# Kernel optimization log

Hardware: AMD Instinct MI355X
Metric: run time of the kernel (lower is better)

Reference implementation:

```python
import jax, jax.numpy as jnp
import numpy as np

EPS = 1e-6

def setup_inputs() -> dict:
    key = jax.random.key(0)
    k1, k2, k3 = jax.random.split(key, 3)
    N, L, S, H, D = 8, 4096, 4096, 8, 64
    queries = jax.random.normal(k1, (N, L, H, D), dtype=jnp.float32)
    keys = jax.random.normal(k2, (N, S, H, D), dtype=jnp.float32)
    values = jax.random.normal(k3, (N, S, H, D), dtype=jnp.float32)
    return {"queries": queries, "keys": keys, "values": values}

def reference(queries, keys, values):
    # elu(x)+1 feature maps (positive kernel)
    Q = jax.nn.elu(queries) + 1.0  # [N,L,H,D]
    K = jax.nn.elu(keys) + 1.0     # [N,S,H,D]
    v_length = values.shape[1]
    v = values / v_length          # scale for numerical stability
    # per-head KV state: [N,H,D,Dv]
    KV = jnp.einsum('nshd,nshv->nhdv', K, v)
    # normalizer: [N,L,H]
    K_sum = K.sum(axis=1)  # [N,H,D]
    Z = 1.0 / (jnp.einsum('nlhd,nhd->nlh', Q, K_sum) + EPS)
    out = jnp.einsum('nlhd,nhdv,nlh->nlhv', Q, KV, Z) * v_length
    return out
```

## Files before the change

### kernel.cpp

```cpp
#include <hip/hip_runtime.h>
#include <hip/hip_bf16.h>
#include <cstddef>
#include <cstdint>

#define N_B   8
#define L_L   4096
#define S_S   4096
#define H_H   8
#define D_D   64
#define NH    64
#define KVLD  68
#define KVSZ  (65 * KVLD)

typedef const float __attribute__((address_space(1)))* gas_fp;
typedef float __attribute__((address_space(3)))* las_fp;

__device__ __forceinline__ float elu1(float x) {
    return x > 0.f ? x + 1.f : __expf(x);
}

__global__ __launch_bounds__(256, 4)
void la_phase1(const float* __restrict__ Kin, const float* __restrict__ Vin,
               float* __restrict__ partials, int split, int schunk)
{
    __shared__ union {
        struct { float K[32 * 64]; float V[2][32 * 64]; } st;
        float acc[64 * 68];
    } sm;
    __shared__ float sKsumP[4 * 64];

    const int b     = blockIdx.x;
    const int nh    = b / split;
    const int chunk = b - nh * split;
    const int n     = nh >> 3;
    const int h     = nh & 7;
    const int s0    = chunk * schunk;

    const int tid  = threadIdx.x;
    const int w    = tid >> 6;
    const int lane = tid & 63;
    const int dg   = lane >> 3;
    const int vg   = lane & 7;

    float acc[8][8];
    #pragma unroll
    for (int i = 0; i < 8; ++i)
        #pragma unroll
        for (int j = 0; j < 8; ++j) acc[i][j] = 0.f;
    float ksum = 0.f;

    const int kd = lane;

    const int lrow = lane >> 4;
    const int lcol = (lane & 15) * 4;

    const float* Kb = Kin + (size_t)n * S_S * (H_H * D_D) + h * D_D;
    const float* Vb = Vin + (size_t)n * S_S * (H_H * D_D) + h * D_D;

    const int ntiles = schunk >> 5;

    #pragma unroll
    for (int c = 0; c < 2; ++c) {
        const int r = w * 8 + c * 4 + lrow;
        __builtin_amdgcn_global_load_lds(
            (gas_fp)(Vb + (size_t)(s0 + r) * (H_H * D_D) + lcol),
            (las_fp)&sm.st.V[0][(w * 8 + c * 4) * 64], 16, 0, 0);
    }

    for (int t = 0; t < ntiles; ++t) {
        const int srow = s0 + t * 32;

        #pragma unroll
        for (int c = 0; c < 2; ++c) {
            const int r = w * 8 + c * 4 + lrow;
            float4 kv = *(const float4*)(Kb + (size_t)(srow + r) * (H_H * D_D) + lcol);
            kv.x = elu1(kv.x); kv.y = elu1(kv.y);
            kv.z = elu1(kv.z); kv.w = elu1(kv.w);
            *(float4*)&sm.st.K[(w * 8 + c * 4) * 64 + lane * 4] = kv;
        }

        if (t + 1 < ntiles) {
            const int srn = srow + 32;
            #pragma unroll
            for (int c = 0; c < 2; ++c) {
                const int r = w * 8 + c * 4 + lrow;
                __builtin_amdgcn_global_load_lds(
                    (gas_fp)(Vb + (size_t)(srn + r) * (H_H * D_D) + lcol),
                    (las_fp)&sm.st.V[(t & 1) ^ 1][(w * 8 + c * 4) * 64], 16, 0, 0);
            }
            asm volatile("s_waitcnt vmcnt(2)" ::: "memory");
        } else {
            asm volatile("s_waitcnt vmcnt(0)" ::: "memory");
        }

        const float* Kbuf = sm.st.K;
        const float* Vbuf = sm.st.V[t & 1];

        #pragma unroll
        for (int sl = 0; sl < 8; ++sl) {
            const int s = w * 8 + sl;
            const float4 k0 = *(const float4*)&Kbuf[s * 64 + dg * 8];
            const float4 k1 = *(const float4*)&Kbuf[s * 64 + dg * 8 + 4];
            const float4 v0 = *(const float4*)&Vbuf[s * 64 + vg * 8];
            const float4 v1 = *(const float4*)&Vbuf[s * 64 + vg * 8 + 4];
            const float kf[8] = {k0.x, k0.y, k0.z, k0.w, k1.x, k1.y, k1.z, k1.w};
            const float vf[8] = {v0.x, v0.y, v0.z, v0.w, v1.x, v1.y, v1.z, v1.w};
            #pragma unroll
            for (int i = 0; i < 8; ++i)
                #pragma unroll
                for (int j = 0; j < 8; ++j)
                    acc[i][j] = fmaf(kf[i], vf[j], acc[i][j]);
        }
        #pragma unroll
        for (int sl = 0; sl < 8; ++sl)
            ksum += Kbuf[(w * 8 + sl) * 64 + kd];
    }
    __syncthreads();

    for (int ww = 0; ww < 4; ++ww) {
        if (w == ww) {
            #pragma unroll
            for (int i = 0; i < 8; ++i) {
                float* p = &sm.acc[(dg * 8 + i) * 68 + vg * 8];
                if (ww == 0) {
                    *(float4*)p       = make_float4(acc[i][0], acc[i][1], acc[i][2], acc[i][3]);
                    *(float4*)(p + 4) = make_float4(acc[i][4], acc[i][5], acc[i][6], acc[i][7]);
                } else {
                    float4 a0 = *(const float4*)p;
                    float4 a1 = *(const float4*)(p + 4);
                    a0.x += acc[i][0]; a0.y += acc[i][1]; a0.z += acc[i][2]; a0.w += acc[i][3];
                    a1.x += acc[i][4]; a1.y += acc[i][5]; a1.z += acc[i][6]; a1.w += acc[i][7];
                    *(float4*)p       = a0;
                    *(float4*)(p + 4) = a1;
                }
            }
        }
        __syncthreads();
    }

    sKsumP[w * 64 + kd] = ksum;
    __syncthreads();

    float* outp = partials + (size_t)b * KVSZ;
    for (int idx = tid; idx < KVSZ; idx += 256) {
        const int r = idx / KVLD;
        const int c = idx - r * KVLD;
        float val = 0.f;
        if (c < 64) {
            if (r < 64)
                val = sm.acc[idx];
            else
                val = sKsumP[c] + sKsumP[64 + c] + sKsumP[128 + c] + sKsumP[192 + c];
        }
        outp[idx] = val;
    }
}

__global__ __launch_bounds__(256)
void la_reduce(const float* __restrict__ partials, float* __restrict__ kvt, int split)
{
    const int idx = blockIdx.x * 256 + threadIdx.x;
    if (idx >= NH * KVSZ) return;
    const int nh  = idx / KVSZ;
    const int rem = idx - nh * KVSZ;
    const float* p = partials + (size_t)nh * split * KVSZ + rem;
    float s = 0.f;
    for (int c = 0; c < split; ++c) s += p[(size_t)c * KVSZ];
    kvt[idx] = s;
}

__global__ __launch_bounds__(256, 2)
void la_phase2(const float* __restrict__ Qin, const float* __restrict__ kvt,
               float* __restrict__ Out)
{
    __shared__ float sQ[128 * 68];
    __shared__ float sKV[KVSZ];

    const int b   = blockIdx.x;
    const int nh  = b >> 5;
    const int lc  = b & 31;
    const int n   = nh >> 3;
    const int h   = nh & 7;
    const int tid = threadIdx.x;
    const int w    = tid >> 6;
    const int lane = tid & 63;

    const float* Qc = Qin + (((size_t)n * L_L + (size_t)lc * 128) * H_H + h) * D_D;
    float*       Oc = Out + (((size_t)n * L_L + (size_t)lc * 128) * H_H + h) * D_D;

    {
        const float4* src = (const float4*)(kvt + (size_t)nh * KVSZ);
        float4*       dst = (float4*)sKV;
        #pragma unroll
        for (int it = 0; it < 4; ++it)
            dst[it * 256 + tid] = src[it * 256 + tid];
        if (tid < 81) dst[1024 + tid] = src[1024 + tid];
    }

    #pragma unroll
    for (int it = 0; it < 8; ++it) {
        const int slot = it * 256 + tid;
        const int r    = slot >> 4;
        const int c4   = slot & 15;
        float4 v = *(const float4*)(Qc + (size_t)r * (H_H * D_D) + c4 * 4);
        v.x = elu1(v.x); v.y = elu1(v.y); v.z = elu1(v.z); v.w = elu1(v.w);
        *(float4*)&sQ[r * 68 + c4 * 4] = v;
    }
    __syncthreads();

    const int rt   = (w >> 1) * 64;
    const int wc   = w & 1;
    const int rl   = lane & 7;
    const int cg   = lane >> 3;
    const int ccol = wc * 32 + cg * 4;

    float acc[8][4];
    float den[8];
    #pragma unroll
    for (int j = 0; j < 8; ++j) {
        den[j] = 0.f;
        #pragma unroll
        for (int m = 0; m < 4; ++m) acc[j][m] = 0.f;
    }

    const int qbase = rt + rl;

    for (int kc = 0; kc < 16; ++kc) {
        float4 qv[8];
        #pragma unroll
        for (int j = 0; j < 8; ++j)
            qv[j] = *(const float4*)&sQ[(qbase + 8 * j) * 68 + kc * 4];
        const float4 kv0 = *(const float4*)&sKV[(kc * 4 + 0) * KVLD + ccol];
        const float4 kv1 = *(const float4*)&sKV[(kc * 4 + 1) * KVLD + ccol];
        const float4 kv2 = *(const float4*)&sKV[(kc * 4 + 2) * KVLD + ccol];
        const float4 kv3 = *(const float4*)&sKV[(kc * 4 + 3) * KVLD + ccol];
        const float4 ks  = *(const float4*)&sKV[64 * KVLD + kc * 4];

        #pragma unroll
        for (int j = 0; j < 8; ++j) {
            const float q0 = qv[j].x, q1 = qv[j].y, q2 = qv[j].z, q3 = qv[j].w;
            den[j] = fmaf(q0, ks.x, den[j]);
            den[j] = fmaf(q1, ks.y, den[j]);
            den[j] = fmaf(q2, ks.z, den[j]);
            den[j] = fmaf(q3, ks.w, den[j]);
            acc[j][0] = fmaf(q0, kv0.x, acc[j][0]);
            acc[j][0] = fmaf(q1, kv1.x, acc[j][0]);
            acc[j][0] = fmaf(q2, kv2.x, acc[j][0]);
            acc[j][0] = fmaf(q3, kv3.x, acc[j][0]);
            acc[j][1] = fmaf(q0, kv0.y, acc[j][1]);
            acc[j][1] = fmaf(q1, kv1.y, acc[j][1]);
            acc[j][1] = fmaf(q2, kv2.y, acc[j][1]);
            acc[j][1] = fmaf(q3, kv3.y, acc[j][1]);
            acc[j][2] = fmaf(q0, kv0.z, acc[j][2]);
            acc[j][2] = fmaf(q1, kv1.z, acc[j][2]);
            acc[j][2] = fmaf(q2, kv2.z, acc[j][2]);
            acc[j][2] = fmaf(q3, kv3.z, acc[j][2]);
            acc[j][3] = fmaf(q0, kv0.w, acc[j][3]);
            acc[j][3] = fmaf(q1, kv1.w, acc[j][3]);
            acc[j][3] = fmaf(q2, kv2.w, acc[j][3]);
            acc[j][3] = fmaf(q3, kv3.w, acc[j][3]);
        }
    }

    #pragma unroll
    for (int j = 0; j < 8; ++j) {
        const float rz = 1.0f / (den[j] + 1e-6f);
        *(float4*)(Oc + (size_t)(qbase + 8 * j) * (H_H * D_D) + ccol) =
            make_float4(acc[j][0] * rz, acc[j][1] * rz,
                        acc[j][2] * rz, acc[j][3] * rz);
    }
}

extern "C" void kernel_launch(void* const* d_in, const int* in_sizes, int n_in,
                              void* d_out, int out_size, void* d_ws, size_t ws_size,
                              hipStream_t stream)
{
    const float* Q = (const float*)d_in[0];
    const float* K = (const float*)d_in[1];
    const float* V = (const float*)d_in[2];
    float* out = (float*)d_out;

    float* kvt = (float*)d_ws;
    const size_t kvt_bytes = (size_t)NH * KVSZ * sizeof(float);

    int split = 16;
    while (split > 1 &&
           kvt_bytes + (size_t)NH * split * KVSZ * sizeof(float) > ws_size)
        split >>= 1;
    float* partials = kvt + (size_t)NH * KVSZ;
    const int schunk = S_S / split;

    la_phase1<<<NH * split, 256, 0, stream>>>(K, V, partials, split, schunk);

    const int red_blocks = (NH * KVSZ + 255) / 256;
    la_reduce<<<red_blocks, 256, 0, stream>>>(partials, kvt, split);

    la_phase2<<<NH * (L_L / 128), 256, 0, stream>>>(Q, kvt, out);
}
```

Measured before the change: 97.18 us.

## Double-buffer K and V via async global-to-LDS loads with in-LDS ELU fixup

K tiles are now loaded asynchronously into LDS with global_load_lds, the same way V already was, instead of through registers with a synchronous load. Both K and V are double-buffered, and the loop is unrolled by two so the next tile's loads overlap the current tile's FMA work. The ELU transform is applied in place in LDS after the load wait. This is meant to hide K load latency. It adds LDS footprint (four 8KB buffers), an extra LDS read-modify-write per tile, and assumes an even tile count.

After: 313.9 us. +223.0%, slower.

```diff
diff --git a/kernel.cpp b/kernel.cpp
--- a/kernel.cpp
+++ b/kernel.cpp
@@ -11,6 +11,7 @@
 #define NH    64
 #define KVLD  68
 #define KVSZ  (65 * KVLD)
+#define TSTRIDE (32 * H_H * D_D)
 
 typedef const float __attribute__((address_space(1)))* gas_fp;
 typedef float __attribute__((address_space(3)))* las_fp;
@@ -24,7 +25,8 @@
                float* __restrict__ partials, int split, int schunk)
 {
     __shared__ union {
-        struct { float K[32 * 64]; float V[2][32 * 64]; } st;
+        struct { float K0[32 * 64]; float K1[32 * 64];
+                 float V0[32 * 64]; float V1[32 * 64]; } st;
         float acc[64 * 68];
     } sm;
     __shared__ float sKsumP[4 * 64];
@@ -54,67 +56,84 @@
     const int lrow = lane >> 4;
     const int lcol = (lane & 15) * 4;
 
-    const float* Kb = Kin + (size_t)n * S_S * (H_H * D_D) + h * D_D;
-    const float* Vb = Vin + (size_t)n * S_S * (H_H * D_D) + h * D_D;
+    const size_t base = (size_t)n * S_S * (H_H * D_D) + h * D_D;
+    const float* kp0 = Kin + base + (size_t)(s0 + w * 8 + 0 + lrow) * (H_H * D_D) + lcol;
+    const float* kp1 = Kin + base + (size_t)(s0 + w * 8 + 4 + lrow) * (H_H * D_D) + lcol;
+    const float* vp0 = Vin + base + (size_t)(s0 + w * 8 + 0 + lrow) * (H_H * D_D) + lcol;
+    const float* vp1 = Vin + base + (size_t)(s0 + w * 8 + 4 + lrow) * (H_H * D_D) + lcol;
 
     const int ntiles = schunk >> 5;
-
-    #pragma unroll
-    for (int c = 0; c < 2; ++c) {
-        const int r = w * 8 + c * 4 + lrow;
-        __builtin_amdgcn_global_load_lds(
-            (gas_fp)(Vb + (size_t)(s0 + r) * (H_H * D_D) + lcol),
-            (las_fp)&sm.st.V[0][(w * 8 + c * 4) * 64], 16, 0, 0);
-    }
-
-    for (int t = 0; t < ntiles; ++t) {
-        const int srow = s0 + t * 32;
-
-        #pragma unroll
-        for (int c = 0; c < 2; ++c) {
-            const int r = w * 8 + c * 4 + lrow;
-            float4 kv = *(const float4*)(Kb + (size_t)(srow + r) * (H_H * D_D) + lcol);
-            kv.x = elu1(kv.x); kv.y = elu1(kv.y);
-            kv.z = elu1(kv.z); kv.w = elu1(kv.w);
-            *(float4*)&sm.st.K[(w * 8 + c * 4) * 64 + lane * 4] = kv;
-        }
-
-        if (t + 1 < ntiles) {
-            const int srn = srow + 32;
-            #pragma unroll
-            for (int c = 0; c < 2; ++c) {
-                const int r = w * 8 + c * 4 + lrow;
-                __builtin_amdgcn_global_load_lds(
-                    (gas_fp)(Vb + (size_t)(srn + r) * (H_H * D_D) + lcol),
-                    (las_fp)&sm.st.V[(t & 1) ^ 1][(w * 8 + c * 4) * 64], 16, 0, 0);
-            }
-            asm volatile("s_waitcnt vmcnt(2)" ::: "memory");
+    const int nt2    = ntiles >> 1;
+
+    const int kb0 = (w * 8 + 0) * 64;
+    const int kb1 = (w * 8 + 4) * 64;
+
+#define ISSUE_TILE(KB, VB)                                                       \
+    do {                                                                         \
+        __builtin_amdgcn_global_load_lds((gas_fp)kp0, (las_fp)&KB[kb0], 16, 0, 0); \
+        __builtin_amdgcn_global_load_lds((gas_fp)kp1, (las_fp)&KB[kb1], 16, 0, 0); \
+        __builtin_amdgcn_global_load_lds((gas_fp)vp0, (las_fp)&VB[kb0], 16, 0, 0); \
+        __builtin_amdgcn_global_load_lds((gas_fp)vp1, (las_fp)&VB[kb1], 16, 0, 0); \
+        kp0 += TSTRIDE; kp1 += TSTRIDE; vp0 += TSTRIDE; vp1 += TSTRIDE;          \
+    } while (0)
+
+#define FIXUP_K(KB)                                                              \
+    do {                                                                         \
+        float* p0_ = &KB[kb0 + lane * 4];                                        \
+        float4 a_ = *(const float4*)p0_;                                         \
+        a_.x = elu1(a_.x); a_.y = elu1(a_.y); a_.z = elu1(a_.z); a_.w = elu1(a_.w); \
+        *(float4*)p0_ = a_;                                                      \
+        float* p1_ = &KB[kb1 + lane * 4];                                        \
+        float4 b_ = *(const float4*)p1_;                                         \
+        b_.x = elu1(b_.x); b_.y = elu1(b_.y); b_.z = elu1(b_.z); b_.w = elu1(b_.w); \
+        *(float4*)p1_ = b_;                                                      \
+    } while (0)
+
+#define COMPUTE_TILE(KB, VB)                                                     \
+    do {                                                                         \
+        _Pragma("unroll")                                                        \
+        for (int sl = 0; sl < 8; ++sl) {                                         \
+            const int s_ = w * 8 + sl;                                           \
+            const float4 k0_ = *(const float4*)&KB[s_ * 64 + dg * 8];            \
+            const float4 k1_ = *(const float4*)&KB[s_ * 64 + dg * 8 + 4];        \
+            const float4 v0_ = *(const float4*)&VB[s_ * 64 + vg * 8];            \
+            const float4 v1_ = *(const float4*)&VB[s_ * 64 + vg * 8 + 4];        \
+            const float kf_[8] = {k0_.x, k0_.y, k0_.z, k0_.w,                    \
+                                  k1_.x, k1_.y, k1_.z, k1_.w};                   \
+            const float vf_[8] = {v0_.x, v0_.y, v0_.z, v0_.w,                    \
+                                  v1_.x, v1_.y, v1_.z, v1_.w};                   \
+            _Pragma("unroll")                                                    \
+            for (int i = 0; i < 8; ++i)                                          \
+                _Pragma("unroll")                                                \
+                for (int j = 0; j < 8; ++j)                                      \
+                    acc[i][j] = fmaf(kf_[i], vf_[j], acc[i][j]);                 \
+        }                                                                        \
+        _Pragma("unroll")                                                        \
+        for (int sl = 0; sl < 8; ++sl)                                           \
+            ksum += KB[(w * 8 + sl) * 64 + kd];                                  \
+    } while (0)
+
+    ISSUE_TILE(sm.st.K0, sm.st.V0);
+
+    for (int tt = 0; tt < nt2; ++tt) {
+        ISSUE_TILE(sm.st.K1, sm.st.V1);
+        asm volatile("s_waitcnt vmcnt(4)" ::: "memory");
+        FIXUP_K(sm.st.K0);
+        COMPUTE_TILE(sm.st.K0, sm.st.V0);
+
+        if (tt + 1 < nt2) {
+            ISSUE_TILE(sm.st.K0, sm.st.V0);
+            asm volatile("s_waitcnt vmcnt(4)" ::: "memory");
         } else {
             asm volatile("s_waitcnt vmcnt(0)" ::: "memory");
         }
-
-        const float* Kbuf = sm.st.K;
-        const float* Vbuf = sm.st.V[t & 1];
-
-        #pragma unroll
-        for (int sl = 0; sl < 8; ++sl) {
-            const int s = w * 8 + sl;
-            const float4 k0 = *(const float4*)&Kbuf[s * 64 + dg * 8];
-            const float4 k1 = *(const float4*)&Kbuf[s * 64 + dg * 8 + 4];
-            const float4 v0 = *(const float4*)&Vbuf[s * 64 + vg * 8];
-            const float4 v1 = *(const float4*)&Vbuf[s * 64 + vg * 8 + 4];
-            const float kf[8] = {k0.x, k0.y, k0.z, k0.w, k1.x, k1.y, k1.z, k1.w};
-            const float vf[8] = {v0.x, v0.y, v0.z, v0.w, v1.x, v1.y, v1.z, v1.w};
-            #pragma unroll
-            for (int i = 0; i < 8; ++i)
-                #pragma unroll
-                for (int j = 0; j < 8; ++j)
-                    acc[i][j] = fmaf(kf[i], vf[j], acc[i][j]);
-        }
-        #pragma unroll
-        for (int sl = 0; sl < 8; ++sl)
-            ksum += Kbuf[(w * 8 + sl) * 64 + kd];
-    }
+        FIXUP_K(sm.st.K1);
+        COMPUTE_TILE(sm.st.K1, sm.st.V1);
+    }
+#undef ISSUE_TILE
+#undef FIXUP_K
+#undef COMPUTE_TILE
+
     __syncthreads();
 
     for (int ww = 0; ww < 4; ++ww) {
```

## Prefetch next K tile into registers during compute in phase1 loop

Applied to the files above, without the earlier changes.

The K tile for the next iteration is now loaded into registers before the current tile's outer-product compute, and the ELU transform plus LDS store happen after compute. Previously each K load sat exposed at the top of the loop. Sched barriers keep the compiler from moving the loads past the compute. Launch bounds are relaxed from 4 to 2 blocks per CU so the extra live registers fit, which may lower occupancy.

New measurement: 99.33 us. 2.2% more time.

```diff
diff --git a/kernel.cpp b/kernel.cpp
--- a/kernel.cpp
+++ b/kernel.cpp
@@ -19,7 +19,7 @@
     return x > 0.f ? x + 1.f : __expf(x);
 }
 
-__global__ __launch_bounds__(256, 4)
+__global__ __launch_bounds__(256, 2)
 void la_phase1(const float* __restrict__ Kin, const float* __restrict__ Vin,
                float* __restrict__ partials, int split, int schunk)
 {
@@ -59,62 +59,76 @@
 
     const int ntiles = schunk >> 5;
 
-    #pragma unroll
-    for (int c = 0; c < 2; ++c) {
-        const int r = w * 8 + c * 4 + lrow;
-        __builtin_amdgcn_global_load_lds(
-            (gas_fp)(Vb + (size_t)(s0 + r) * (H_H * D_D) + lcol),
-            (las_fp)&sm.st.V[0][(w * 8 + c * 4) * 64], 16, 0, 0);
+    float4 ka0, ka1;
+
+#define ELU4(X) do { X.x = elu1(X.x); X.y = elu1(X.y); \
+                     X.z = elu1(X.z); X.w = elu1(X.w); } while (0)
+
+    {
+        #pragma unroll
+        for (int c = 0; c < 2; ++c) {
+            __builtin_amdgcn_global_load_lds(
+                (gas_fp)(Vb + (size_t)(s0 + w * 8 + c * 4 + lrow) * (H_H * D_D) + lcol),
+                (las_fp)&sm.st.V[0][(w * 8 + c * 4) * 64], 16, 0, 0);
+        }
+        ka0 = *(const float4*)(Kb + (size_t)(s0 + w * 8 + 0 + lrow) * (H_H * D_D) + lcol);
+        ka1 = *(const float4*)(Kb + (size_t)(s0 + w * 8 + 4 + lrow) * (H_H * D_D) + lcol);
+        asm volatile("s_waitcnt vmcnt(0)" ::: "memory");
+        ELU4(ka0); ELU4(ka1);
+        *(float4*)&sm.st.K[(w * 8 + 0) * 64 + lane * 4] = ka0;
+        *(float4*)&sm.st.K[(w * 8 + 4) * 64 + lane * 4] = ka1;
     }
 
     for (int t = 0; t < ntiles; ++t) {
-        const int srow = s0 + t * 32;
-
-        #pragma unroll
-        for (int c = 0; c < 2; ++c) {
-            const int r = w * 8 + c * 4 + lrow;
-            float4 kv = *(const float4*)(Kb + (size_t)(srow + r) * (H_H * D_D) + lcol);
-            kv.x = elu1(kv.x); kv.y = elu1(kv.y);
-            kv.z = elu1(kv.z); kv.w = elu1(kv.w);
-            *(float4*)&sm.st.K[(w * 8 + c * 4) * 64 + lane * 4] = kv;
-        }
-
-        if (t + 1 < ntiles) {
-            const int srn = srow + 32;
+        const bool more = (t + 1 < ntiles);
+
+        if (more) {
+            const int srn = s0 + (t + 1) * 32;
+            float* vdst = sm.st.V[(t + 1) & 1];
             #pragma unroll
             for (int c = 0; c < 2; ++c) {
-                const int r = w * 8 + c * 4 + lrow;
                 __builtin_amdgcn_global_load_lds(
-                    (gas_fp)(Vb + (size_t)(srn + r) * (H_H * D_D) + lcol),
-                    (las_fp)&sm.st.V[(t & 1) ^ 1][(w * 8 + c * 4) * 64], 16, 0, 0);
+                    (gas_fp)(Vb + (size_t)(srn + w * 8 + c * 4 + lrow) * (H_H * D_D) + lcol),
+                    (las_fp)&vdst[(w * 8 + c * 4) * 64], 16, 0, 0);
             }
-            asm volatile("s_waitcnt vmcnt(2)" ::: "memory");
-        } else {
+            ka0 = *(const float4*)(Kb + (size_t)(srn + w * 8 + 0 + lrow) * (H_H * D_D) + lcol);
+            ka1 = *(const float4*)(Kb + (size_t)(srn + w * 8 + 4 + lrow) * (H_H * D_D) + lcol);
+        }
+        __builtin_amdgcn_sched_barrier(0);
+
+        {
+            const float* Kbuf = sm.st.K;
+            const float* Vbuf = sm.st.V[t & 1];
+            #pragma unroll
+            for (int sl = 0; sl < 8; ++sl) {
+                const int s = w * 8 + sl;
+                const float4 k0 = *(const float4*)&Kbuf[s * 64 + dg * 8];
+                const float4 k1 = *(const float4*)&Kbuf[s * 64 + dg * 8 + 4];
+                const float4 v0 = *(const float4*)&Vbuf[s * 64 + vg * 8];
+                const float4 v1 = *(const float4*)&Vbuf[s * 64 + vg * 8 + 4];
+                const float kf[8] = {k0.x, k0.y, k0.z, k0.w, k1.x, k1.y, k1.z, k1.w};
+                const float vf[8] = {v0.x, v0.y, v0.z, v0.w, v1.x, v1.y, v1.z, v1.w};
+                #pragma unroll
+                for (int i = 0; i < 8; ++i)
+                    #pragma unroll
+                    for (int j = 0; j < 8; ++j)
+                        acc[i][j] = fmaf(kf[i], vf[j], acc[i][j]);
+            }
+            #pragma unroll
+            for (int sl = 0; sl < 8; ++sl)
+                ksum += Kbuf[(w * 8 + sl) * 64 + kd];
+        }
+        __builtin_amdgcn_sched_barrier(0);
+
+        if (more) {
             asm volatile("s_waitcnt vmcnt(0)" ::: "memory");
-        }
-
-        const float* Kbuf = sm.st.K;
-        const float* Vbuf = sm.st.V[t & 1];
-
-        #pragma unroll
-        for (int sl = 0; sl < 8; ++sl) {
-            const int s = w * 8 + sl;
-            const float4 k0 = *(const float4*)&Kbuf[s * 64 + dg * 8];
-            const float4 k1 = *(const float4*)&Kbuf[s * 64 + dg * 8 + 4];
-            const float4 v0 = *(const float4*)&Vbuf[s * 64 + vg * 8];
-            const float4 v1 = *(const float4*)&Vbuf[s * 64 + vg * 8 + 4];
-            const float kf[8] = {k0.x, k0.y, k0.z, k0.w, k1.x, k1.y, k1.z, k1.w};
-            const float vf[8] = {v0.x, v0.y, v0.z, v0.w, v1.x, v1.y, v1.z, v1.w};
-            #pragma unroll
-            for (int i = 0; i < 8; ++i)
-                #pragma unroll
-                for (int j = 0; j < 8; ++j)
-                    acc[i][j] = fmaf(kf[i], vf[j], acc[i][j]);
-        }
-        #pragma unroll
-        for (int sl = 0; sl < 8; ++sl)
-            ksum += Kbuf[(w * 8 + sl) * 64 + kd];
-    }
+            ELU4(ka0); ELU4(ka1);
+            *(float4*)&sm.st.K[(w * 8 + 0) * 64 + lane * 4] = ka0;
+            *(float4*)&sm.st.K[(w * 8 + 4) * 64 + lane * 4] = ka1;
+        }
+    }
+#undef ELU4
+
     __syncthreads();
 
     for (int ww = 0; ww < 4; ++ww) {
```
